# Performance work log

Measured on AMD Instinct MI355X. Metric: run time of the kernel, lower is better.

The kernel has to match this reference:

```python
import jax, jax.numpy as jnp
import numpy as np

N = 20000      # nodes
E = 640000     # edges
H = 128        # hidden_channels
F = 128        # num_filters
G = 50         # num_gaussians
L = 6          # num_interactions
CUT = 10.0     # cutoff
NG = 64        # num graphs in batch
NODE_CLASS = 100


def ssp(x):
    # ShiftedSoftplus: softplus(x) - log(2)
    return jax.nn.softplus(x) - jnp.asarray(np.log(2.0), x.dtype)


def setup_inputs() -> dict:
    key = jax.random.key(0)
    ks = jax.random.split(key, 20)
    z = jax.random.randint(ks[0], (N,), 0, NODE_CLASS)
    pos = jax.random.normal(ks[1], (N, 3), dtype=jnp.float32) * 3.0
    edge_index = jax.random.randint(ks[2], (2, E), 0, N)
    batch = jnp.sort(jax.random.randint(ks[3], (N,), 0, NG))
    s = 0.05
    emb = jax.random.normal(ks[4], (NODE_CLASS, H), dtype=jnp.float32) * s
    mlp_w1 = jax.random.normal(ks[5], (L, G, F), dtype=jnp.float32) * s
    mlp_b1 = jnp.zeros((L, F), jnp.float32)
    mlp_w2 = jax.random.normal(ks[6], (L, F, F), dtype=jnp.float32) * s
    mlp_b2 = jnp.zeros((L, F), jnp.float32)
    conv_w1 = jax.random.normal(ks[7], (L, H, F), dtype=jnp.float32) * s
    conv_w2 = jax.random.normal(ks[8], (L, F, H), dtype=jnp.float32) * s
    conv_b2 = jnp.zeros((L, H), jnp.float32)
    lin_w = jax.random.normal(ks[9], (L, H, H), dtype=jnp.float32) * s
    lin_b = jnp.zeros((L, H), jnp.float32)
    out1_w = jax.random.normal(ks[10], (H, H), dtype=jnp.float32) * s
    out1_b = jnp.zeros((H,), jnp.float32)
    out2_w = jax.random.normal(ks[11], (H, H), dtype=jnp.float32) * s
    out2_b = jnp.zeros((H,), jnp.float32)
    return dict(z=z, pos=pos, edge_index=edge_index, batch=batch, emb=emb,
                mlp_w1=mlp_w1, mlp_b1=mlp_b1, mlp_w2=mlp_w2, mlp_b2=mlp_b2,
                conv_w1=conv_w1, conv_w2=conv_w2, conv_b2=conv_b2,
                lin_w=lin_w, lin_b=lin_b,
                out1_w=out1_w, out1_b=out1_b, out2_w=out2_w, out2_b=out2_b)


def reference(z, pos, edge_index, batch, emb,
              mlp_w1, mlp_b1, mlp_w2, mlp_b2,
              conv_w1, conv_w2, conv_b2, lin_w, lin_b,
              out1_w, out1_b, out2_w, out2_b):
    src, dst = edge_index[0], edge_index[1]  # x_j = x[src], aggregate at dst
    h = emb[z]                               # [N, H]
    d = jnp.linalg.norm(pos[src] - pos[dst], axis=-1)  # [E]
    # GaussianSmearing(0, cutoff, G)
    offset = jnp.linspace(0.0, CUT, G).astype(d.dtype)
    coeff = -0.5 / (offset[1] - offset[0]) ** 2
    edge_attr = jnp.exp(coeff * (d[:, None] - offset[None, :]) ** 2)  # [E, G]
    # cosine cutoff
    C = 0.5 * (jnp.cos(d * jnp.pi / CUT) + 1.0)  # [E]
    n = h.shape[0]
    for l in range(L):
        # edge filter: mlp(edge_attr) * C
        W = ssp(edge_attr @ mlp_w1[l] + mlp_b1[l]) @ mlp_w2[l] + mlp_b2[l]
        W = W * C[:, None]                      # [E, F]
        xf = h @ conv_w1[l]                     # lin1, no bias: [N, F]
        msg = xf[src] * W                       # gather + weight
        agg = jax.ops.segment_sum(msg, dst, num_segments=n)  # scatter-add
        x = agg @ conv_w2[l] + conv_b2[l]       # lin2
        x = ssp(x)
        x = x @ lin_w[l] + lin_b[l]
        h = h + x                               # residual
    h = ssp(h @ out1_w + out1_b) @ out2_w + out2_b
    # readout = 'mean'
    sums = jax.ops.segment_sum(h, batch, num_segments=NG)
    cnt = jax.ops.segment_sum(jnp.ones((n,), h.dtype), batch, num_segments=NG)
    return sums / jnp.maximum(cnt, 1.0)[:, None]
```

## Files before the change

kernel.cpp:

```cpp
#include <hip/hip_runtime.h>
#include <math.h>

#define NN 20000
#define NE 640000
#define GDIM 50
#define LAYERS 6
#define NGRAPH 64
#define TBL 2048
#define DMAXF 12.8f
#define G2_PAD 136

typedef __attribute__((ext_vector_type(8))) short short8;
typedef __attribute__((ext_vector_type(4))) float floatx4;

__device__ __forceinline__ float sspf(float x) {
    float sp = (x > 30.0f) ? x : log1pf(expf(x));
    return sp - 0.69314718055994530942f;
}

__device__ __forceinline__ unsigned short f2bs(float f) {
    union { float f; unsigned int i; } u; u.f = f;
    unsigned int r = u.i + 0x7fffu + ((u.i >> 16) & 1u);
    return (unsigned short)(r >> 16);
}

__device__ __forceinline__ float bs2f(unsigned int bits16) {
    union { unsigned int i; float f; } u; u.i = bits16 << 16;
    return u.f;
}

__device__ __forceinline__ short8 pack_bf16x8(float4 a, float4 b) {
    short8 o;
    o[0] = (short)f2bs(a.x); o[1] = (short)f2bs(a.y);
    o[2] = (short)f2bs(a.z); o[3] = (short)f2bs(a.w);
    o[4] = (short)f2bs(b.x); o[5] = (short)f2bs(b.y);
    o[6] = (short)f2bs(b.z); o[7] = (short)f2bs(b.w);
    return o;
}

__global__ void init_misc(int* __restrict__ deg, float* __restrict__ out,
                          float* __restrict__ A) {
    int idx = blockIdx.x * blockDim.x + threadIdx.x;
    if (idx < NN) { deg[idx] = 0; return; }
    int j = idx - NN;
    if (j < NGRAPH * 128) { out[j] = 0.f; return; }
    j -= NGRAPH * 128;
    const int total = (TBL + 2) * GDIM;
    if (j >= total) return;
    int i = j / GDIM, g = j % GDIM;
    float v = 0.0f;
    if (i <= TBL) {
        float d = (float)i * (DMAXF / (float)TBL);
        float step = 10.0f / 49.0f;
        float off = (float)g * step;
        float coeff = -0.5f / (step * step);
        float dd = d - off;
        v = expf(coeff * dd * dd);
    }
    A[j] = v;
}

__global__ void deg_hist(const int* __restrict__ dst, int* __restrict__ deg) {
    int j = blockIdx.x * blockDim.x + threadIdx.x;
    if (j >= NE) return;
    atomicAdd(&deg[dst[j]], 1);
}

__global__ void scan_deg(const int* __restrict__ deg, int* __restrict__ row_ptr,
                         int* __restrict__ cursor) {
    __shared__ int part[1024];
    const int n = NN;
    const int PER = 20;
    int t = threadIdx.x;
    int base = t * PER;
    int local[PER];
    int s = 0;
    #pragma unroll
    for (int i = 0; i < PER; i++) {
        int k = base + i;
        local[i] = s;
        if (k < n) s += deg[k];
    }
    part[t] = s;
    __syncthreads();
    for (int off = 1; off < 1024; off <<= 1) {
        int v = (t >= off) ? part[t - off] : 0;
        __syncthreads();
        part[t] += v;
        __syncthreads();
    }
    int offset = (t > 0) ? part[t - 1] : 0;
    #pragma unroll
    for (int i = 0; i < PER; i++) {
        int k = base + i;
        if (k <= n) {
            int v = offset + local[i];
            row_ptr[k] = v;
            if (k < n) cursor[k] = v;
        }
    }
}

__global__ void csr_fill(const float* __restrict__ pos, const int* __restrict__ src,
                         const int* __restrict__ dst, int* __restrict__ cursor,
                         int2* __restrict__ csr) {
    int j = blockIdx.x * blockDim.x + threadIdx.x;
    if (j >= NE) return;
    int s = src[j], tno = dst[j];
    float dx = pos[3*s+0] - pos[3*tno+0];
    float dy = pos[3*s+1] - pos[3*tno+1];
    float dz = pos[3*s+2] - pos[3*tno+2];
    float d = sqrtf(dx*dx + dy*dy + dz*dz);
    float u = d * ((float)TBL / DMAXF);
    u = fminf(u, (float)(TBL + 1));
    int i0 = (int)u; if (i0 > TBL) i0 = TBL;
    float f = u - (float)i0;
    int p = atomicAdd(&cursor[tno], 1);
    csr[p] = make_int2((i0 << 15) | s, __float_as_int(f));
}

template <int K>
__launch_bounds__(256, 2)
__global__ void gemm_t(const float* __restrict__ A, const float* __restrict__ W,
                       const float* __restrict__ bias, float* __restrict__ Y, int M,
                       int act, int aStride, int wStride, int bStride, int yStride) {
    constexpr int KP = (K + 3) & ~3;
    __shared__ __align__(16) float Ws[KP * 128];
    __shared__ __align__(16) float As[32 * KP];
    int l = blockIdx.y;
    A += (size_t)l * aStride;
    W += (size_t)l * wStride;
    if (bias) bias += (size_t)l * bStride;
    Y += (size_t)l * yStride;
    int t = threadIdx.x;
    int row0 = blockIdx.x * 32;
    for (int i = t; i < KP * 128; i += 256) Ws[i] = (i < K * 128) ? W[i] : 0.0f;
    for (int i = t; i < 32 * KP; i += 256) {
        int r = i / KP, k = i % KP;
        float v = 0.f;
        if (k < K && row0 + r < M) v = A[(size_t)(row0 + r) * K + k];
        As[r * KP + k] = v;
    }
    __syncthreads();
    int tx = t & 31, ty = t >> 5;
    int c0 = tx * 4, r0 = ty * 4;
    float acc[4][4] = {{0.f}};
    #pragma unroll 4
    for (int k = 0; k < KP; k += 4) {
        float4 a0 = *(const float4*)&As[(r0 + 0) * KP + k];
        float4 a1 = *(const float4*)&As[(r0 + 1) * KP + k];
        float4 a2 = *(const float4*)&As[(r0 + 2) * KP + k];
        float4 a3 = *(const float4*)&As[(r0 + 3) * KP + k];
        float4 w0 = *(const float4*)&Ws[(k + 0) * 128 + c0];
        float4 w1 = *(const float4*)&Ws[(k + 1) * 128 + c0];
        float4 w2 = *(const float4*)&Ws[(k + 2) * 128 + c0];
        float4 w3 = *(const float4*)&Ws[(k + 3) * 128 + c0];
        float av[4][4] = {{a0.x,a0.y,a0.z,a0.w},{a1.x,a1.y,a1.z,a1.w},
                          {a2.x,a2.y,a2.z,a2.w},{a3.x,a3.y,a3.z,a3.w}};
        float wv[4][4] = {{w0.x,w0.y,w0.z,w0.w},{w1.x,w1.y,w1.z,w1.w},
                          {w2.x,w2.y,w2.z,w2.w},{w3.x,w3.y,w3.z,w3.w}};
        #pragma unroll
        for (int i = 0; i < 4; i++)
            #pragma unroll
            for (int j = 0; j < 4; j++)
                #pragma unroll
                for (int q = 0; q < 4; q++)
                    acc[i][j] += av[i][q] * wv[q][j];
    }
    float b0 = 0.f, b1 = 0.f, b2 = 0.f, b3 = 0.f;
    if (bias) { b0 = bias[c0]; b1 = bias[c0+1]; b2 = bias[c0+2]; b3 = bias[c0+3]; }
    #pragma unroll
    for (int i = 0; i < 4; i++) {
        int r = row0 + r0 + i;
        if (r >= M) break;
        float4 v;
        v.x = acc[i][0] + b0; v.y = acc[i][1] + b1; v.z = acc[i][2] + b2; v.w = acc[i][3] + b3;
        if (act == 1) { v.x = sspf(v.x); v.y = sspf(v.y); v.z = sspf(v.z); v.w = sspf(v.w); }
        *(float4*)&Y[(size_t)r * 128 + c0] = v;
    }
}

struct WArgs { const float* s[26]; unsigned short* d[26]; };
__global__ void wprep_all(WArgs a) {
    __shared__ float tile[32][33];
    int mz = blockIdx.z;
    const float* Wm = a.s[mz];
    unsigned short* Wo = a.d[mz];
    int bx = blockIdx.x * 32, by = blockIdx.y * 32;
    int tx = threadIdx.x & 31, ty = threadIdx.x >> 5;
    for (int r = ty; r < 32; r += 8) tile[r][tx] = Wm[(by + r) * 128 + bx + tx];
    __syncthreads();
    for (int r = ty; r < 32; r += 8) Wo[(bx + r) * 128 + by + tx] = f2bs(tile[tx][r]);
}

__launch_bounds__(256)
__global__ void gemm_cs(const float* __restrict__ A, const unsigned short* __restrict__ Wt,
                        const float* __restrict__ bias,
                        float* __restrict__ Yf, unsigned short* __restrict__ Yb,
                        int M, int act,
                        int aStride, int wStride, int bStride, int yStride) {
    int l = blockIdx.y;
    A += (size_t)l * aStride;
    Wt += (size_t)l * wStride;
    if (bias) bias += (size_t)l * bStride;
    if (Yf) Yf += (size_t)l * yStride;
    if (Yb) Yb += (size_t)l * yStride;
    int wv = threadIdx.x >> 6, lane = threadIdx.x & 63;
    int row0 = blockIdx.x * 32;
    if (row0 >= M) return;
    int lm = lane & 15, lk = (lane >> 4) * 8, orow = (lane >> 4) * 4;
    int r0 = row0 + lm;      r0 = (r0 < M) ? r0 : M - 1;
    int r1 = row0 + 16 + lm; r1 = (r1 < M) ? r1 : M - 1;
    const float* Ap0 = A + (size_t)r0 * 128;
    const float* Ap1 = A + (size_t)r1 * 128;
    short8 af0[4], af1[4];
    #pragma unroll
    for (int kq = 0; kq < 4; kq++) {
        af0[kq] = pack_bf16x8(*(const float4*)(Ap0 + kq * 32 + lk),
                              *(const float4*)(Ap0 + kq * 32 + lk + 4));
        af1[kq] = pack_bf16x8(*(const float4*)(Ap1 + kq * 32 + lk),
                              *(const float4*)(Ap1 + kq * 32 + lk + 4));
    }
    floatx4 acc[2][2];
    #pragma unroll
    for (int i = 0; i < 2; i++)
        #pragma unroll
        for (int j = 0; j < 2; j++) acc[i][j] = (floatx4){0, 0, 0, 0};
    const unsigned short* Wp = Wt + (size_t)(wv * 32) * 128;
    #pragma unroll
    for (int kq = 0; kq < 4; kq++) {
        #pragma unroll
        for (int ct = 0; ct < 2; ct++) {
            short8 bf = *(const short8*)(Wp + (size_t)(ct * 16 + lm) * 128 + kq * 32 + lk);
            acc[0][ct] = __builtin_amdgcn_mfma_f32_16x16x32_bf16(af0[kq], bf, acc[0][ct], 0, 0, 0);
            acc[1][ct] = __builtin_amdgcn_mfma_f32_16x16x32_bf16(af1[kq], bf, acc[1][ct], 0, 0, 0);
        }
    }
    #pragma unroll
    for (int tt = 0; tt < 2; tt++) {
        #pragma unroll
        for (int ct = 0; ct < 2; ct++) {
            int c = wv * 32 + ct * 16 + lm;
            float b = bias ? bias[c] : 0.f;
            #pragma unroll
            for (int r = 0; r < 4; r++) {
                int rr = row0 + tt * 16 + orow + r;
                if (rr >= M) continue;
                float v = acc[tt][ct][r] + b;
                if (act) v = sspf(v);
                if (Yf) Yf[(size_t)rr * 128 + c] = v;
                if (Yb) Yb[(size_t)rr * 128 + c] = f2bs(v);
            }
        }
    }
}

__launch_bounds__(256)
__global__ void gemm3(const float* __restrict__ A,
                      const unsigned short* __restrict__ W2t, const float* __restrict__ b2,
                      const unsigned short* __restrict__ W3t, const float* __restrict__ b3,
                      const float* __restrict__ resid, float* __restrict__ Yf,
                      const unsigned short* __restrict__ W1nt, unsigned short* __restrict__ xfb) {
    __shared__ unsigned short Ls[16 * G2_PAD];
    int wv = threadIdx.x >> 6, lane = threadIdx.x & 63;
    int row0 = blockIdx.x * 16;
    int lm = lane & 15, lk = (lane >> 4) * 8, orow = (lane >> 4) * 4;
    int cw = wv * 32;
    {
        const float* Ap = A + (size_t)(row0 + lm) * 128;
        short8 af[4];
        #pragma unroll
        for (int kq = 0; kq < 4; kq++)
            af[kq] = pack_bf16x8(*(const float4*)(Ap + kq * 32 + lk),
                                 *(const float4*)(Ap + kq * 32 + lk + 4));
        floatx4 acc[2];
        acc[0] = (floatx4){0, 0, 0, 0}; acc[1] = (floatx4){0, 0, 0, 0};
        const unsigned short* Wp = W2t + (size_t)cw * 128;
        #pragma unroll
        for (int kq = 0; kq < 4; kq++) {
            #pragma unroll
            for (int ct = 0; ct < 2; ct++) {
                short8 bf = *(const short8*)(Wp + (size_t)(ct * 16 + lm) * 128 + kq * 32 + lk);
                acc[ct] = __builtin_amdgcn_mfma_f32_16x16x32_bf16(af[kq], bf, acc[ct], 0, 0, 0);
            }
        }
        #pragma unroll
        for (int ct = 0; ct < 2; ct++) {
            int c = cw + ct * 16 + lm;
            float b = b2[c];
            #pragma unroll
            for (int r = 0; r < 4; r++)
                Ls[(orow + r) * G2_PAD + c] = f2bs(sspf(acc[ct][r] + b));
        }
    }
    __syncthreads();
    float vout[2][4];
    {
        short8 a2[4];
        #pragma unroll
        for (int kq = 0; kq < 4; kq++)
            a2[kq] = *(const short8*)&Ls[lm * G2_PAD + kq * 32 + lk];
        floatx4 acc[2];
        acc[0] = (floatx4){0, 0, 0, 0}; acc[1] = (floatx4){0, 0, 0, 0};
        const unsigned short* Wp = W3t + (size_t)cw * 128;
        #pragma unroll
        for (int kq = 0; kq < 4; kq++) {
            #pragma unroll
            for (int ct = 0; ct < 2; ct++) {
                short8 bf = *(const short8*)(Wp + (size_t)(ct * 16 + lm) * 128 + kq * 32 + lk);
                acc[ct] = __builtin_amdgcn_mfma_f32_16x16x32_bf16(a2[kq], bf, acc[ct], 0, 0, 0);
            }
        }
        #pragma unroll
        for (int ct = 0; ct < 2; ct++) {
            int c = cw + ct * 16 + lm;
            float b = b3[c];
            #pragma unroll
            for (int r = 0; r < 4; r++) {
                int rr = row0 + orow + r;
                float v = acc[ct][r] + b;
                if (resid) v += resid[(size_t)rr * 128 + c];
                Yf[(size_t)rr * 128 + c] = v;
                vout[ct][r] = v;
            }
        }
    }
    if (!W1nt) return;
    __syncthreads();
    #pragma unroll
    for (int ct = 0; ct < 2; ct++) {
        int c = cw + ct * 16 + lm;
        #pragma unroll
        for (int r = 0; r < 4; r++)
            Ls[(orow + r) * G2_PAD + c] = f2bs(vout[ct][r]);
    }
    __syncthreads();
    {
        short8 a3[4];
        #pragma unroll
        for (int kq = 0; kq < 4; kq++)
            a3[kq] = *(const short8*)&Ls[lm * G2_PAD + kq * 32 + lk];
        floatx4 acc[2];
        acc[0] = (floatx4){0, 0, 0, 0}; acc[1] = (floatx4){0, 0, 0, 0};
        const unsigned short* Wp = W1nt + (size_t)cw * 128;
        #pragma unroll
        for (int kq = 0; kq < 4; kq++) {
            #pragma unroll
            for (int ct = 0; ct < 2; ct++) {
                short8 bf = *(const short8*)(Wp + (size_t)(ct * 16 + lm) * 128 + kq * 32 + lk);
                acc[ct] = __builtin_amdgcn_mfma_f32_16x16x32_bf16(a3[kq], bf, acc[ct], 0, 0, 0);
            }
        }
        #pragma unroll
        for (int ct = 0; ct < 2; ct++) {
            int c = cw + ct * 16 + lm;
            #pragma unroll
            for (int r = 0; r < 4; r++)
                xfb[(size_t)(row0 + orow + r) * 128 + c] = f2bs(acc[ct][r]);
        }
    }
}

__global__ void tquant(const float* __restrict__ T, unsigned int* __restrict__ Tb) {
    int idx = blockIdx.x * blockDim.x + threadIdx.x;
    const int total = LAYERS * (TBL + 1) * 128;
    if (idx >= total) return;
    int c = idx & 127;
    int li = idx >> 7;
    int i = li % (TBL + 1);
    int l = li / (TBL + 1);
    float d0 = (float)i * (DMAXF / (float)TBL);
    float d1 = (float)(i + 1) * (DMAXF / (float)TBL);
    float C0 = 0.5f * (cosf(d0 * 0.31415926535897931f) + 1.0f);
    float C1 = 0.5f * (cosf(d1 * 0.31415926535897931f) + 1.0f);
    const float* row = T + ((size_t)l * (TBL + 2) + i) * 128 + c;
    float w = row[0] * C0;
    float nw = row[128] * C1;
    Tb[idx] = ((unsigned)f2bs(nw - w) << 16) | f2bs(w);
}

__global__ void h_init(const int* __restrict__ z, const float* __restrict__ emb,
                       float* __restrict__ h) {
    int idx = blockIdx.x * blockDim.x + threadIdx.x;
    if (idx >= NN * 32) return;
    int n = idx >> 5, q = idx & 31;
    ((float4*)h)[n * 32 + q] = ((const float4*)emb)[z[n] * 32 + q];
}

__launch_bounds__(256)
__global__ void edge_agg(const int* __restrict__ row_ptr, const int2* __restrict__ csr,
                         const unsigned int* __restrict__ Tb,
                         const unsigned short* __restrict__ xfb,
                         float* __restrict__ agg) {
    int wv = __builtin_amdgcn_readfirstlane(threadIdx.x >> 6);
    int lane = threadIdx.x & 63;
    int n = blockIdx.x * 2 + (wv >> 1);
    if (n >= NN) return;
    int c = (wv & 1) * 64 + lane;
    int e0 = row_ptr[n], e1 = row_ptr[n + 1];
    float ax = 0.f;
    int e = e0;
    for (; e + 8 <= e1; e += 8) {
        int2 ed[8];
        #pragma unroll
        for (int q = 0; q < 8; q++) ed[q] = csr[e + q];
        unsigned int tw[8]; unsigned short xv[8];
        #pragma unroll
        for (int q = 0; q < 8; q++) {
            unsigned int px = (unsigned int)ed[q].x;
            tw[q] = Tb[(px >> 15) * 128 + c];
            xv[q] = xfb[(size_t)(px & 0x7fffu) * 128 + c];
        }
        #pragma unroll
        for (int q = 0; q < 8; q++) {
            float f = __int_as_float(ed[q].y);
            float w = bs2f(tw[q] & 0xffffu), dw = bs2f(tw[q] >> 16);
            float x = bs2f((unsigned int)xv[q]);
            ax = fmaf(x, fmaf(f, dw, w), ax);
        }
    }
    for (; e < e1; e++) {
        int2 ed = csr[e];
        unsigned int px = (unsigned int)ed.x;
        unsigned int tw = Tb[(px >> 15) * 128 + c];
        unsigned short xv = xfb[(size_t)(px & 0x7fffu) * 128 + c];
        float f = __int_as_float(ed.y);
        float w = bs2f(tw & 0xffffu), dw = bs2f(tw >> 16);
        float x = bs2f((unsigned int)xv);
        ax = fmaf(x, fmaf(f, dw, w), ax);
    }
    agg[(size_t)n * 128 + c] = ax;
}

#define RCHUNK 32
__global__ void raccum(const float* __restrict__ hout, const int* __restrict__ batch,
                       float* __restrict__ out) {
    int b = blockIdx.x, c = threadIdx.x;
    int n0 = b * RCHUNK;
    if (n0 >= NN) return;
    int n1 = n0 + RCHUNK; if (n1 > NN) n1 = NN;
    int g = batch[n0];
    float s = 0.f;
    for (int n = n0; n < n1; n++) {
        int bg = batch[n];
        if (bg != g) { atomicAdd(&out[g * 128 + c], s); s = 0.f; g = bg; }
        s += hout[(size_t)n * 128 + c];
    }
    atomicAdd(&out[g * 128 + c], s);
}

__global__ void rdiv(const int* __restrict__ batch, float* __restrict__ out) {
    int g = blockIdx.x;
    int c = threadIdx.x;
    __shared__ int sh[2];
    if (c < 2) {
        int target = g + c;
        int lo = 0, hi = NN;
        while (lo < hi) {
            int mid = (lo + hi) >> 1;
            if (batch[mid] < target) lo = mid + 1; else hi = mid;
        }
        sh[c] = lo;
    }
    __syncthreads();
    int cnt = sh[1] - sh[0];
    out[g * 128 + c] /= (float)(cnt > 0 ? cnt : 1);
}

extern "C" void kernel_launch(void* const* d_in, const int* in_sizes, int n_in,
                              void* d_out, int out_size, void* d_ws, size_t ws_size,
                              hipStream_t stream) {
    const int*   z       = (const int*)d_in[0];
    const float* pos     = (const float*)d_in[1];
    const int*   eidx    = (const int*)d_in[2];
    const int*   src     = eidx;
    const int*   dst     = eidx + NE;
    const int*   batch   = (const int*)d_in[3];
    const float* emb     = (const float*)d_in[4];
    const float* mlp_w1  = (const float*)d_in[5];
    const float* mlp_b1  = (const float*)d_in[6];
    const float* mlp_w2  = (const float*)d_in[7];
    const float* mlp_b2  = (const float*)d_in[8];
    const float* conv_w1 = (const float*)d_in[9];
    const float* conv_w2 = (const float*)d_in[10];
    const float* conv_b2 = (const float*)d_in[11];
    const float* lin_w   = (const float*)d_in[12];
    const float* lin_b   = (const float*)d_in[13];
    const float* out1_w  = (const float*)d_in[14];
    const float* out1_b  = (const float*)d_in[15];
    const float* out2_w  = (const float*)d_in[16];
    const float* out2_b  = (const float*)d_in[17];
    float* out = (float*)d_out;

    char* wp = (char*)d_ws;
    auto alloc = [&](size_t bytes) {
        char* p = wp;
        wp += (bytes + 255) & ~(size_t)255;
        return p;
    };
    const int Mt = TBL + 2;
    int*    deg     = (int*)alloc(NN * 4);
    int*    row_ptr = (int*)alloc((NN + 1) * 4);
    int*    cursor  = (int*)alloc(NN * 4);
    int2*   csr     = (int2*)alloc((size_t)NE * 8);
    float*  A_tab   = (float*)alloc((size_t)Mt * GDIM * 4);
    float*  T1all   = (float*)alloc((size_t)LAYERS * Mt * 128 * 4);
    float*  T       = (float*)alloc((size_t)LAYERS * Mt * 128 * 4);
    unsigned int* Tb = (unsigned int*)alloc((size_t)LAYERS * (TBL + 1) * 128 * 4);
    float*  h       = (float*)alloc((size_t)NN * 128 * 4);
    float*  agg     = (float*)alloc((size_t)NN * 128 * 4);
    unsigned short* xfb = (unsigned short*)alloc((size_t)NN * 128 * 2);
    unsigned short* wbf = (unsigned short*)alloc((size_t)26 * 16384 * 2);
    unsigned short* mlp_w2t  = wbf;
    unsigned short* conv_w1t = wbf + (size_t)6 * 16384;
    unsigned short* conv_w2t = wbf + (size_t)12 * 16384;
    unsigned short* lin_wt   = wbf + (size_t)18 * 16384;
    unsigned short* out1_wt  = wbf + (size_t)24 * 16384;
    unsigned short* out2_wt  = wbf + (size_t)25 * 16384;

    const int initN = NN + NGRAPH * 128 + Mt * GDIM;
    init_misc<<<(initN + 255) / 256, 256, 0, stream>>>(deg, out, A_tab);

    deg_hist<<<(NE + 255) / 256, 256, 0, stream>>>(dst, deg);
    scan_deg<<<1, 1024, 0, stream>>>(deg, row_ptr, cursor);
    csr_fill<<<(NE + 255) / 256, 256, 0, stream>>>(pos, src, dst, cursor, csr);

    WArgs wa;
    for (int l = 0; l < 6; l++) {
        wa.s[l]      = mlp_w2  + (size_t)l * 16384;  wa.d[l]      = mlp_w2t  + (size_t)l * 16384;
        wa.s[6 + l]  = conv_w1 + (size_t)l * 16384;  wa.d[6 + l]  = conv_w1t + (size_t)l * 16384;
        wa.s[12 + l] = conv_w2 + (size_t)l * 16384;  wa.d[12 + l] = conv_w2t + (size_t)l * 16384;
        wa.s[18 + l] = lin_w   + (size_t)l * 16384;  wa.d[18 + l] = lin_wt   + (size_t)l * 16384;
    }
    wa.s[24] = out1_w; wa.d[24] = out1_wt;
    wa.s[25] = out2_w; wa.d[25] = out2_wt;
    wprep_all<<<dim3(4, 4, 26), 256, 0, stream>>>(wa);

    const int gt32 = (Mt + 31) / 32;
    gemm_t<GDIM><<<dim3(gt32, LAYERS), 256, 0, stream>>>(
        A_tab, mlp_w1, mlp_b1, T1all, Mt, 1, 0, GDIM * 128, 128, Mt * 128);
    gemm_cs<<<dim3(gt32, LAYERS), 256, 0, stream>>>(
        T1all, mlp_w2t, mlp_b2, T, nullptr, Mt, 0,
        Mt * 128, 16384, 128, Mt * 128);
    tquant<<<(LAYERS * (TBL + 1) * 128 + 255) / 256, 256, 0, stream>>>(T, Tb);

    h_init<<<(NN * 32 + 255) / 256, 256, 0, stream>>>(z, emb, h);
    gemm_cs<<<NN / 32, 256, 0, stream>>>(h, conv_w1t, nullptr, nullptr, xfb, NN, 0, 0, 0, 0, 0);

    const int gn = NN / 16;
    for (int l = 0; l < LAYERS; l++) {
        edge_agg<<<NN / 2, 256, 0, stream>>>(row_ptr, csr,
                                             Tb + (size_t)l * (TBL + 1) * 128,
                                             xfb, agg);
        const unsigned short* w1n = (l + 1 < LAYERS) ? conv_w1t + (size_t)(l + 1) * 16384 : nullptr;
        gemm3<<<gn, 256, 0, stream>>>(agg, conv_w2t + (size_t)l * 16384, conv_b2 + l * 128,
                                      lin_wt + (size_t)l * 16384, lin_b + l * 128,
                                      h, h, w1n, xfb);
    }

    gemm3<<<gn, 256, 0, stream>>>(h, out1_wt, out1_b, out2_wt, out2_b,
                                  nullptr, agg, nullptr, nullptr);

    raccum<<<(NN + RCHUNK - 1) / RCHUNK, 128, 0, stream>>>(agg, batch, out);
    rdiv<<<NGRAPH, 128, 0, stream>>>(batch, out);
}
```

Before: 621.0 us.

## Merge setup kernels, parallelize degree scan, and widen edge aggregation unroll

Folds the weight transpose, init and embedding-gather kernels into one launch. It replaces the single-block degree scan with a two-pass multi-block scan and merges the table GEMM with the first xf GEMM into one grid. Edge aggregation now loads 16 edges at a time, moves CSR entries into scalar registers with readfirstlane, and adds a 4-edge tail loop. The goal is to cut launch count and serial setup latency and to improve memory-level parallelism in the gather. In exchange, the merged GEMM grid launches many empty blocks for the table part, and the wider unroll raises register pressure.

```diff
diff --git a/kernel.cpp b/kernel.cpp
--- a/kernel.cpp
+++ b/kernel.cpp
@@ -38,26 +38,48 @@
     return o;
 }
 
-__global__ void init_misc(int* __restrict__ deg, float* __restrict__ out,
-                          float* __restrict__ A) {
-    int idx = blockIdx.x * blockDim.x + threadIdx.x;
+struct WArgs { const float* s[26]; unsigned short* d[26]; };
+#define PREP_WBLK 416
+__global__ void prep_a(WArgs a, int* __restrict__ deg, float* __restrict__ out,
+                       float* __restrict__ A_tab, const int* __restrict__ z,
+                       const float* __restrict__ emb, float* __restrict__ h) {
+    __shared__ float tile[32][33];
+    int b = blockIdx.x;
+    if (b < PREP_WBLK) {
+        int mz = b >> 4, sub = b & 15;
+        int bx = (sub & 3) * 32, by = (sub >> 2) * 32;
+        const float* Wm = a.s[mz];
+        unsigned short* Wo = a.d[mz];
+        int tx = threadIdx.x & 31, ty = threadIdx.x >> 5;
+        for (int r = ty; r < 32; r += 8) tile[r][tx] = Wm[(by + r) * 128 + bx + tx];
+        __syncthreads();
+        for (int r = ty; r < 32; r += 8) Wo[(bx + r) * 128 + by + tx] = f2bs(tile[tx][r]);
+        return;
+    }
+    int idx = (b - PREP_WBLK) * 256 + threadIdx.x;
     if (idx < NN) { deg[idx] = 0; return; }
-    int j = idx - NN;
-    if (j < NGRAPH * 128) { out[j] = 0.f; return; }
-    j -= NGRAPH * 128;
-    const int total = (TBL + 2) * GDIM;
-    if (j >= total) return;
-    int i = j / GDIM, g = j % GDIM;
-    float v = 0.0f;
-    if (i <= TBL) {
-        float d = (float)i * (DMAXF / (float)TBL);
-        float step = 10.0f / 49.0f;
-        float off = (float)g * step;
-        float coeff = -0.5f / (step * step);
-        float dd = d - off;
-        v = expf(coeff * dd * dd);
-    }
-    A[j] = v;
+    idx -= NN;
+    if (idx < NGRAPH * 128) { out[idx] = 0.f; return; }
+    idx -= NGRAPH * 128;
+    if (idx < (TBL + 2) * GDIM) {
+        int i = idx / GDIM, g = idx % GDIM;
+        float v = 0.0f;
+        if (i <= TBL) {
+            float d = (float)i * (DMAXF / (float)TBL);
+            float step = 10.0f / 49.0f;
+            float off = (float)g * step;
+            float coeff = -0.5f / (step * step);
+            float dd = d - off;
+            v = expf(coeff * dd * dd);
+        }
+        A_tab[idx] = v;
+        return;
+    }
+    idx -= (TBL + 2) * GDIM;
+    if (idx < NN * 32) {
+        int n = idx >> 5, q = idx & 31;
+        ((float4*)h)[n * 32 + q] = ((const float4*)emb)[(size_t)z[n] * 32 + q];
+    }
 }
 
 __global__ void deg_hist(const int* __restrict__ dst, int* __restrict__ deg) {
@@ -66,39 +88,46 @@
     atomicAdd(&deg[dst[j]], 1);
 }
 
-__global__ void scan_deg(const int* __restrict__ deg, int* __restrict__ row_ptr,
-                         int* __restrict__ cursor) {
-    __shared__ int part[1024];
-    const int n = NN;
-    const int PER = 20;
-    int t = threadIdx.x;
-    int base = t * PER;
-    int local[PER];
-    int s = 0;
-    #pragma unroll
-    for (int i = 0; i < PER; i++) {
-        int k = base + i;
-        local[i] = s;
-        if (k < n) s += deg[k];
-    }
-    part[t] = s;
+__global__ void scan_a(const int* __restrict__ deg, int* __restrict__ row_ptr,
+                       int* __restrict__ bsum) {
+    __shared__ int sh[256];
+    int b = blockIdx.x, t = threadIdx.x;
+    int i = b * 256 + t;
+    int v = (i < NN) ? deg[i] : 0;
+    int x = v;
+    sh[t] = x;
     __syncthreads();
-    for (int off = 1; off < 1024; off <<= 1) {
-        int v = (t >= off) ? part[t - off] : 0;
+    for (int off = 1; off < 256; off <<= 1) {
+        int u = (t >= off) ? sh[t - off] : 0;
         __syncthreads();
-        part[t] += v;
+        x += u;
+        sh[t] = x;
         __syncthreads();
     }
-    int offset = (t > 0) ? part[t - 1] : 0;
-    #pragma unroll
-    for (int i = 0; i < PER; i++) {
-        int k = base + i;
-        if (k <= n) {
-            int v = offset + local[i];
-            row_ptr[k] = v;
-            if (k < n) cursor[k] = v;
-        }
-    }
+    if (i <= NN) row_ptr[i] = x - v;
+    if (t == 255) bsum[b] = x;
+}
+
+__global__ void scan_b(const int* __restrict__ bsum, int* __restrict__ row_ptr,
+                       int* __restrict__ cursor) {
+    __shared__ int spref;
+    int b = blockIdx.x, t = threadIdx.x;
+    if (t < 64) {
+        int s = 0;
+        if (t < b) s += bsum[t];
+        if (t + 64 < b) s += bsum[t + 64];
+        for (int off = 32; off; off >>= 1) s += __shfl_down(s, off);
+        if (t == 0) spref = s;
+    }
+    __syncthreads();
+    int prefix = spref;
+    int i = b * 256 + t;
+    if (i < NN) {
+        int v = row_ptr[i] + prefix;
+        row_ptr[i] = v;
+        cursor[i] = v;
+    }
+    if (b == 0 && t == 0) row_ptr[NN] = NE;
 }
 
 __global__ void csr_fill(const float* __restrict__ pos, const int* __restrict__ src,
@@ -180,31 +209,24 @@
     }
 }
 
-struct WArgs { const float* s[26]; unsigned short* d[26]; };
-__global__ void wprep_all(WArgs a) {
-    __shared__ float tile[32][33];
-    int mz = blockIdx.z;
-    const float* Wm = a.s[mz];
-    unsigned short* Wo = a.d[mz];
-    int bx = blockIdx.x * 32, by = blockIdx.y * 32;
-    int tx = threadIdx.x & 31, ty = threadIdx.x >> 5;
-    for (int r = ty; r < 32; r += 8) tile[r][tx] = Wm[(by + r) * 128 + bx + tx];
-    __syncthreads();
-    for (int r = ty; r < 32; r += 8) Wo[(bx + r) * 128 + by + tx] = f2bs(tile[tx][r]);
-}
-
 __launch_bounds__(256)
-__global__ void gemm_cs(const float* __restrict__ A, const unsigned short* __restrict__ Wt,
-                        const float* __restrict__ bias,
-                        float* __restrict__ Yf, unsigned short* __restrict__ Yb,
-                        int M, int act,
-                        int aStride, int wStride, int bStride, int yStride) {
-    int l = blockIdx.y;
-    A += (size_t)l * aStride;
-    Wt += (size_t)l * wStride;
-    if (bias) bias += (size_t)l * bStride;
-    if (Yf) Yf += (size_t)l * yStride;
-    if (Yb) Yb += (size_t)l * yStride;
+__global__ void gemm_cs2(const float* __restrict__ A1, const unsigned short* __restrict__ W1t,
+                         const float* __restrict__ bias1, float* __restrict__ Y1, int M1,
+                         const float* __restrict__ A2, const unsigned short* __restrict__ W2t,
+                         unsigned short* __restrict__ Yb2, int M2) {
+    int y = blockIdx.y;
+    const float* A; const unsigned short* Wt; const float* bias;
+    float* Yf; unsigned short* Yb; int M;
+    if (y < LAYERS) {
+        M = M1;
+        A = A1 + (size_t)y * M1 * 128;
+        Wt = W1t + (size_t)y * 16384;
+        bias = bias1 + (size_t)y * 128;
+        Yf = Y1 + (size_t)y * M1 * 128;
+        Yb = nullptr;
+    } else {
+        M = M2; A = A2; Wt = W2t; bias = nullptr; Yf = nullptr; Yb = Yb2;
+    }
     int wv = threadIdx.x >> 6, lane = threadIdx.x & 63;
     int row0 = blockIdx.x * 32;
     if (row0 >= M) return;
@@ -247,7 +269,6 @@
                 int rr = row0 + tt * 16 + orow + r;
                 if (rr >= M) continue;
                 float v = acc[tt][ct][r] + b;
-                if (act) v = sspf(v);
                 if (Yf) Yf[(size_t)rr * 128 + c] = v;
                 if (Yb) Yb[(size_t)rr * 128 + c] = f2bs(v);
             }
@@ -266,6 +287,14 @@
     int row0 = blockIdx.x * 16;
     int lm = lane & 15, lk = (lane >> 4) * 8, orow = (lane >> 4) * 4;
     int cw = wv * 32;
+    float rpre[2][4];
+    if (resid) {
+        #pragma unroll
+        for (int ct = 0; ct < 2; ct++)
+            #pragma unroll
+            for (int r = 0; r < 4; r++)
+                rpre[ct][r] = resid[(size_t)(row0 + orow + r) * 128 + cw + ct * 16 + lm];
+    }
     {
         const float* Ap = A + (size_t)(row0 + lm) * 128;
         short8 af[4];
@@ -319,7 +348,7 @@
             for (int r = 0; r < 4; r++) {
                 int rr = row0 + orow + r;
                 float v = acc[ct][r] + b;
-                if (resid) v += resid[(size_t)rr * 128 + c];
+                if (resid) v += rpre[ct][r];
                 Yf[(size_t)rr * 128 + c] = v;
                 vout[ct][r] = v;
             }
@@ -379,14 +408,6 @@
     Tb[idx] = ((unsigned)f2bs(nw - w) << 16) | f2bs(w);
 }
 
-__global__ void h_init(const int* __restrict__ z, const float* __restrict__ emb,
-                       float* __restrict__ h) {
-    int idx = blockIdx.x * blockDim.x + threadIdx.x;
-    if (idx >= NN * 32) return;
-    int n = idx >> 5, q = idx & 31;
-    ((float4*)h)[n * 32 + q] = ((const float4*)emb)[z[n] * 32 + q];
-}
-
 __launch_bounds__(256)
 __global__ void edge_agg(const int* __restrict__ row_ptr, const int2* __restrict__ csr,
                          const unsigned int* __restrict__ Tb,
@@ -395,36 +416,58 @@
     int wv = __builtin_amdgcn_readfirstlane(threadIdx.x >> 6);
     int lane = threadIdx.x & 63;
     int n = blockIdx.x * 2 + (wv >> 1);
-    if (n >= NN) return;
     int c = (wv & 1) * 64 + lane;
     int e0 = row_ptr[n], e1 = row_ptr[n + 1];
     float ax = 0.f;
     int e = e0;
-    for (; e + 8 <= e1; e += 8) {
-        int2 ed[8];
-        #pragma unroll
-        for (int q = 0; q < 8; q++) ed[q] = csr[e + q];
-        unsigned int tw[8]; unsigned short xv[8];
-        #pragma unroll
-        for (int q = 0; q < 8; q++) {
-            unsigned int px = (unsigned int)ed[q].x;
-            tw[q] = Tb[(px >> 15) * 128 + c];
-            xv[q] = xfb[(size_t)(px & 0x7fffu) * 128 + c];
-        }
-        #pragma unroll
-        for (int q = 0; q < 8; q++) {
-            float f = __int_as_float(ed[q].y);
+    for (; e + 16 <= e1; e += 16) {
+        unsigned int px[16]; float ff[16];
+        #pragma unroll
+        for (int q = 0; q < 16; q++) {
+            int2 ed = csr[e + q];
+            px[q] = (unsigned int)__builtin_amdgcn_readfirstlane(ed.x);
+            ff[q] = __int_as_float(__builtin_amdgcn_readfirstlane(ed.y));
+        }
+        unsigned int tw[16]; unsigned short xv[16];
+        #pragma unroll
+        for (int q = 0; q < 16; q++) {
+            tw[q] = Tb[(px[q] >> 15) * 128 + c];
+            xv[q] = xfb[(size_t)(px[q] & 0x7fffu) * 128 + c];
+        }
+        #pragma unroll
+        for (int q = 0; q < 16; q++) {
             float w = bs2f(tw[q] & 0xffffu), dw = bs2f(tw[q] >> 16);
             float x = bs2f((unsigned int)xv[q]);
-            ax = fmaf(x, fmaf(f, dw, w), ax);
+            ax = fmaf(x, fmaf(ff[q], dw, w), ax);
+        }
+    }
+    for (; e + 4 <= e1; e += 4) {
+        unsigned int px[4]; float ff[4];
+        #pragma unroll
+        for (int q = 0; q < 4; q++) {
+            int2 ed = csr[e + q];
+            px[q] = (unsigned int)__builtin_amdgcn_readfirstlane(ed.x);
+            ff[q] = __int_as_float(__builtin_amdgcn_readfirstlane(ed.y));
+        }
+        unsigned int tw[4]; unsigned short xv[4];
+        #pragma unroll
+        for (int q = 0; q < 4; q++) {
+            tw[q] = Tb[(px[q] >> 15) * 128 + c];
+            xv[q] = xfb[(size_t)(px[q] & 0x7fffu) * 128 + c];
+        }
+        #pragma unroll
+        for (int q = 0; q < 4; q++) {
+            float w = bs2f(tw[q] & 0xffffu), dw = bs2f(tw[q] >> 16);
+            float x = bs2f((unsigned int)xv[q]);
+            ax = fmaf(x, fmaf(ff[q], dw, w), ax);
         }
     }
     for (; e < e1; e++) {
         int2 ed = csr[e];
-        unsigned int px = (unsigned int)ed.x;
+        unsigned int px = (unsigned int)__builtin_amdgcn_readfirstlane(ed.x);
+        float f = __int_as_float(__builtin_amdgcn_readfirstlane(ed.y));
         unsigned int tw = Tb[(px >> 15) * 128 + c];
         unsigned short xv = xfb[(size_t)(px & 0x7fffu) * 128 + c];
-        float f = __int_as_float(ed.y);
         float w = bs2f(tw & 0xffffu), dw = bs2f(tw >> 16);
         float x = bs2f((unsigned int)xv);
         ax = fmaf(x, fmaf(f, dw, w), ax);
@@ -502,6 +545,7 @@
     int*    deg     = (int*)alloc(NN * 4);
     int*    row_ptr = (int*)alloc((NN + 1) * 4);
     int*    cursor  = (int*)alloc(NN * 4);
+    int*    bsum    = (int*)alloc(128 * 4);
     int2*   csr     = (int2*)alloc((size_t)NE * 8);
     float*  A_tab   = (float*)alloc((size_t)Mt * GDIM * 4);
     float*  T1all   = (float*)alloc((size_t)LAYERS * Mt * 128 * 4);
@@ -518,13 +562,6 @@
     unsigned short* out1_wt  = wbf + (size_t)24 * 16384;
     unsigned short* out2_wt  = wbf + (size_t)25 * 16384;
 
-    const int initN = NN + NGRAPH * 128 + Mt * GDIM;
-    init_misc<<<(initN + 255) / 256, 256, 0, stream>>>(deg, out, A_tab);
-
-    deg_hist<<<(NE + 255) / 256, 256, 0, stream>>>(dst, deg);
-    scan_deg<<<1, 1024, 0, stream>>>(deg, row_ptr, cursor);
-    csr_fill<<<(NE + 255) / 256, 256, 0, stream>>>(pos, src, dst, cursor, csr);
-
     WArgs wa;
     for (int l = 0; l < 6; l++) {
         wa.s[l]      = mlp_w2  + (size_t)l * 16384;  wa.d[l]      = mlp_w2t  + (size_t)l * 16384;
@@ -534,18 +571,22 @@
     }
     wa.s[24] = out1_w; wa.d[24] = out1_wt;
     wa.s[25] = out2_w; wa.d[25] = out2_wt;
-    wprep_all<<<dim3(4, 4, 26), 256, 0, stream>>>(wa);
+    const int initN = NN + NGRAPH * 128 + Mt * GDIM + NN * 32;
+    prep_a<<<PREP_WBLK + (initN + 255) / 256, 256, 0, stream>>>(wa, deg, out, A_tab, z, emb, h);
+
+    deg_hist<<<(NE + 255) / 256, 256, 0, stream>>>(dst, deg);
+    const int NB = (NN + 255) / 256;
+    scan_a<<<NB, 256, 0, stream>>>(deg, row_ptr, bsum);
+    scan_b<<<NB, 256, 0, stream>>>(bsum, row_ptr, cursor);
+    csr_fill<<<(NE + 255) / 256, 256, 0, stream>>>(pos, src, dst, cursor, csr);
 
     const int gt32 = (Mt + 31) / 32;
     gemm_t<GDIM><<<dim3(gt32, LAYERS), 256, 0, stream>>>(
         A_tab, mlp_w1, mlp_b1, T1all, Mt, 1, 0, GDIM * 128, 128, Mt * 128);
-    gemm_cs<<<dim3(gt32, LAYERS), 256, 0, stream>>>(
-        T1all, mlp_w2t, mlp_b2, T, nullptr, Mt, 0,
-        Mt * 128, 16384, 128, Mt * 128);
+    gemm_cs2<<<dim3(NN / 32, LAYERS + 1), 256, 0, stream>>>(
+        T1all, mlp_w2t, mlp_b2, T, Mt,
+        h, conv_w1t, xfb, NN);
     tquant<<<(LAYERS * (TBL + 1) * 128 + 255) / 256, 256, 0, stream>>>(T, Tb);
-
-    h_init<<<(NN * 32 + 255) / 256, 256, 0, stream>>>(z, emb, h);
-    gemm_cs<<<NN / 32, 256, 0, stream>>>(h, conv_w1t, nullptr, nullptr, xfb, NN, 0, 0, 0, 0, 0);
 
     const int gn = NN / 16;
     for (int l = 0; l < LAYERS; l++) {
```

New measurement: 553.4 us. 1.12x faster.
